# Performance work log

Measured on AMD Instinct MI355X. Metric: run time of the kernel, lower is better.

The kernel has to match this reference:

```python
import jax, jax.numpy as jnp
import numpy as np

N_HEADS = 16
DIM = 1024
HEAD_DIM = DIM // N_HEADS

def setup_inputs() -> dict:
    key = jax.random.key(0)
    ks = jax.random.split(key, 5)
    B, S = 4, 2048
    x = jax.random.normal(ks[0], (B, S, DIM), dtype=jnp.float32)
    # PyTorch Linear-style params (stored as [in, out] for x @ W)
    sc = 1.0 / np.sqrt(DIM)
    W_qkv = jax.random.uniform(ks[1], (DIM, 3 * DIM), jnp.float32, -sc, sc)
    b_qkv = jax.random.uniform(ks[2], (3 * DIM,), jnp.float32, -sc, sc)
    W_o = jax.random.uniform(ks[3], (DIM, DIM), jnp.float32, -sc, sc)
    b_o = jax.random.uniform(ks[4], (DIM,), jnp.float32, -sc, sc)
    return {"x": x, "W_qkv": W_qkv, "b_qkv": b_qkv, "W_o": W_o, "b_o": b_o}

def reference(x, W_qkv, b_qkv, W_o, b_o):
    B, S, D = x.shape
    qkv = x @ W_qkv + b_qkv                       # [B,S,3D]
    q, k, v = jnp.split(qkv, 3, axis=2)
    # [B,S,D] -> [B,H,S,hd]
    q = q.reshape(B, S, N_HEADS, HEAD_DIM).transpose(0, 2, 1, 3)
    k = k.reshape(B, S, N_HEADS, HEAD_DIM).transpose(0, 2, 1, 3)
    v = v.reshape(B, S, N_HEADS, HEAD_DIM).transpose(0, 2, 1, 3)
    aff = jnp.einsum('bhqd,bhkd->bhqk', q, k) / jnp.sqrt(jnp.float32(HEAD_DIM))
    causal = jnp.tril(jnp.ones((S, S), dtype=bool))  # [S,S]
    aff = jnp.where(causal[None, None], aff, jnp.float32(-jnp.inf))
    attn = jax.nn.softmax(aff, axis=3)
    # dropout p=0.0 (eval): identity
    out = jnp.einsum('bhqk,bhkd->bhqd', attn, v)
    out = out.transpose(0, 2, 1, 3).reshape(B, S, D)
    return out @ W_o + b_o
```

## Files before the change

### kernel.cpp

```cpp
#include <hip/hip_runtime.h>

typedef unsigned short u16;
typedef short bf16x8 __attribute__((ext_vector_type(8)));
typedef float f32x4 __attribute__((ext_vector_type(4)));
typedef unsigned short ushort8v __attribute__((ext_vector_type(8)));
typedef unsigned short us4 __attribute__((ext_vector_type(4)));
typedef float f4v __attribute__((ext_vector_type(4)));

#define LOG2E 1.4426950408889634f
#define FIXMAX_C (12.0f * LOG2E)

static __device__ __forceinline__ float bf2f(u16 h) {
    unsigned int u = ((unsigned int)h) << 16;
    return __builtin_bit_cast(float, u);
}
static __device__ __forceinline__ u16 f2bf(float f) {
    unsigned int u = __builtin_bit_cast(unsigned int, f);
    u += 0x7FFFu + ((u >> 16) & 1u);
    return (u16)(u >> 16);
}
static __device__ __forceinline__ void ld_lds16(const u16* g, u16* l) {
    __builtin_amdgcn_global_load_lds((const __attribute__((address_space(1))) void*)g,
                                     (__attribute__((address_space(3))) void*)l, 16, 0, 0);
}
#define MFMA16(a, b, c) __builtin_amdgcn_mfma_f32_16x16x32_bf16(a, b, c, 0, 0, 0)
#define SW(r, g) (((r) << 6) + ((((g) ^ ((r) & 7))) << 3))

__global__ void cvt_cast(const float* __restrict__ src, u16* __restrict__ dst, int n4) {
    int i = blockIdx.x * blockDim.x + threadIdx.x;
    const int stride = gridDim.x * blockDim.x;
    for (; i < n4; i += stride) {
        f4v v = *(const f4v*)(src + (size_t)i * 4);
        us4 o;
        o[0] = f2bf(v[0]); o[1] = f2bf(v[1]); o[2] = f2bf(v[2]); o[3] = f2bf(v[3]);
        *(us4*)(dst + (size_t)i * 4) = o;
    }
}

__global__ void cvt_T(const float* __restrict__ W, u16* __restrict__ WT, int N, int K) {
    int idx = blockIdx.x * 256 + threadIdx.x;
    int n = idx % N;
    int k0 = (idx / N) * 4;
    us4 pk;
    #pragma unroll
    for (int j = 0; j < 4; j++) pk[j] = f2bf(W[(size_t)(k0 + j) * N + n]);
    *(us4*)&WT[(size_t)n * K + k0] = pk;
}

template <int MODE>
__global__ __launch_bounds__(256) void gemm128(
        const u16* __restrict__ A, const u16* __restrict__ BT,
        const u16* __restrict__ bias, void* __restrict__ Cout,
        u16* __restrict__ vT, int K) {
    __shared__ u16 As[128 * 32];
    __shared__ u16 Bs[128 * 32];
    const int tid = threadIdx.x, lane = tid & 63, wid = tid >> 6;
    const int lm = lane & 15, q = lane >> 4;
    const int m0 = blockIdx.y * 128, n0 = blockIdx.x * 128;
    const int wm = (wid >> 1) * 64, wn = (wid & 1) * 64;
    f32x4 acc[4][4] = {};

    const int srow = wid * 32 + (lane >> 2);
    const int scol = (lane & 3) * 8;
    const u16* ga0 = A + (size_t)(m0 + srow) * K + scol;
    const u16* ga1 = ga0 + (size_t)16 * K;
    const u16* gb0 = BT + (size_t)(n0 + srow) * K + scol;
    const u16* gb1 = gb0 + (size_t)16 * K;
    u16* lA = &As[wid * 32 * 32];
    u16* lB = &Bs[wid * 32 * 32];

    for (int kb = 0; kb < K; kb += 32) {
        __syncthreads();
        ld_lds16(ga0 + kb, lA);
        ld_lds16(ga1 + kb, lA + 16 * 32);
        ld_lds16(gb0 + kb, lB);
        ld_lds16(gb1 + kb, lB + 16 * 32);
        __syncthreads();
        bf16x8 af[4], bfr[4];
        #pragma unroll
        for (int mi = 0; mi < 4; mi++) af[mi] = *(const bf16x8*)&As[(wm + mi * 16 + lm) * 32 + q * 8];
        #pragma unroll
        for (int ni = 0; ni < 4; ni++) bfr[ni] = *(const bf16x8*)&Bs[(wn + ni * 16 + lm) * 32 + q * 8];
        #pragma unroll
        for (int mi = 0; mi < 4; mi++)
            #pragma unroll
            for (int ni = 0; ni < 4; ni++)
                acc[mi][ni] = MFMA16(af[mi], bfr[ni], acc[mi][ni]);
    }

    if constexpr (MODE == 0) {
        u16* qkout = (u16*)Cout;
        if (n0 < 2048) {
            #pragma unroll
            for (int ni = 0; ni < 4; ni++) {
                int col = n0 + wn + ni * 16 + lm;
                float bsv = bf2f(bias[col]);
                float sc = (col < 1024) ? 0.125f : 1.0f;
                #pragma unroll
                for (int mi = 0; mi < 4; mi++)
                    #pragma unroll
                    for (int r = 0; r < 4; r++) {
                        int row = m0 + wm + mi * 16 + q * 4 + r;
                        qkout[(size_t)row * 2048 + col] = f2bf((acc[mi][ni][r] + bsv) * sc);
                    }
            }
        } else {
            const int b_ = m0 >> 11;
            const int sb = (m0 & 2047) + wm;
            #pragma unroll
            for (int ni = 0; ni < 4; ni++) {
                int col = n0 + wn + ni * 16 + lm;
                int hh = (col - 2048) >> 6, dd = (col - 2048) & 63;
                float bsv = bf2f(bias[col]);
                u16* dst = vT + ((size_t)((b_ * 16 + hh) * 64 + dd)) * 2048;
                #pragma unroll
                for (int mi = 0; mi < 4; mi++) {
                    us4 pk;
                    #pragma unroll
                    for (int r = 0; r < 4; r++) pk[r] = f2bf(acc[mi][ni][r] + bsv);
                    *(us4*)&dst[sb + mi * 16 + q * 4] = pk;
                }
            }
        }
    } else {
        float* out = (float*)Cout;
        #pragma unroll
        for (int ni = 0; ni < 4; ni++) {
            int col = n0 + wn + ni * 16 + lm;
            float bsv = bf2f(bias[col]);
            #pragma unroll
            for (int mi = 0; mi < 4; mi++)
                #pragma unroll
                for (int r = 0; r < 4; r++) {
                    int row = m0 + wm + mi * 16 + q * 4 + r;
                    out[(size_t)row * 1024 + col] = acc[mi][ni][r] + bsv;
                }
        }
    }
}

template <bool DIAG>
__device__ __forceinline__ void proc_tile(
        const bf16x8* qf, const u16* __restrict__ ksv, const u16* __restrict__ vsv,
        u16* __restrict__ psw, f32x4* o, f32x4& lacc, const bf16x8 ones,
        int lm, int q, int m0w) {
    f32x4 s[4] = {};
    #pragma unroll
    for (int g2 = 0; g2 < 2; g2++) {
        bf16x8 a = qf[g2];
        #pragma unroll
        for (int nt = 0; nt < 4; nt++) {
            bf16x8 bb = *(const bf16x8*)&ksv[SW(nt * 16 + lm, q + 4 * g2)];
            s[nt] = MFMA16(a, bb, s[nt]);
        }
    }
    #pragma unroll
    for (int nt = 0; nt < 4; nt++)
        #pragma unroll
        for (int r = 0; r < 4; r++) {
            float v = s[nt][r];
            if constexpr (DIAG) {
                if (nt * 16 + lm > m0w + q * 4 + r) v = -3e30f;
            }
            float pv = __builtin_amdgcn_exp2f(v * LOG2E - FIXMAX_C);
            psw[SW(q * 4 + r, 2 * nt + (lm >> 3)) + (lm & 7)] = f2bf(pv);
        }
    #pragma unroll
    for (int g2 = 0; g2 < 2; g2++) {
        bf16x8 ap = *(const bf16x8*)&psw[SW(lm, q + 4 * g2)];
        lacc = MFMA16(ap, ones, lacc);
        #pragma unroll
        for (int nt = 0; nt < 4; nt++) {
            bf16x8 bv = *(const bf16x8*)&vsv[SW(nt * 16 + lm, q + 4 * g2)];
            o[nt] = MFMA16(ap, bv, o[nt]);
        }
    }
}

__global__ __launch_bounds__(256, 2) void attn3(
        const u16* __restrict__ qk, const u16* __restrict__ vT, u16* __restrict__ aw) {
    __shared__ u16 smem[16384];
    u16* ks = smem;
    u16* vs = smem + 4096;
    const int tid = threadIdx.x, lane = tid & 63, wid = tid >> 6;
    const int lm = lane & 15, q = lane >> 4;
    const int bh = blockIdx.x, p = blockIdx.y;
    const int b = bh >> 4, h = bh & 15;
    const int t[4] = {p, 15 - p, 16 + p, 31 - p};
    const size_t rowbase = (size_t)b * 2048;
    const int lr = tid >> 2, lcg = (tid & 3) * 2, lc = (tid & 3) * 16;
    const int m0w = wid * 16;
    u16* psw = smem + 8192 + wid * 1024;

    bf16x8 ones;
    #pragma unroll
    for (int j = 0; j < 8; j++) ones[j] = (short)0x3F80;

    #pragma unroll
    for (int i = 0; i < 4; i++) {
        const u16* qa = qk + (rowbase + t[i] * 64 + lr) * 2048 + h * 64 + lc;
        *(ushort8v*)&smem[i * 4096 + SW(lr, lcg)]     = *(const ushort8v*)qa;
        *(ushort8v*)&smem[i * 4096 + SW(lr, lcg + 1)] = *(const ushort8v*)(qa + 8);
    }
    __syncthreads();
    bf16x8 qf[4][2];
    #pragma unroll
    for (int i = 0; i < 4; i++)
        #pragma unroll
        for (int g2 = 0; g2 < 2; g2++)
            qf[i][g2] = *(const bf16x8*)&smem[i * 4096 + SW(m0w + lm, q + 4 * g2)];

    f32x4 o[4][4] = {};
    f32x4 lacc[4] = {};

    const u16* kg = qk + (rowbase + lr) * 2048 + 1024 + h * 64 + lc;
    const u16* vg = vT + ((size_t)bh * 64 + lr) * 2048 + lc;
    const int jmax = t[3];

    ushort8v k0 = *(const ushort8v*)kg, k1 = *(const ushort8v*)(kg + 8);
    ushort8v v0 = *(const ushort8v*)vg, v1 = *(const ushort8v*)(vg + 8);

    for (int jt = 0; jt <= jmax; ++jt) {
        __syncthreads();
        *(ushort8v*)&ks[SW(lr, lcg)] = k0; *(ushort8v*)&ks[SW(lr, lcg + 1)] = k1;
        *(ushort8v*)&vs[SW(lr, lcg)] = v0; *(ushort8v*)&vs[SW(lr, lcg + 1)] = v1;
        __syncthreads();
        if (jt < jmax) {
            const u16* kgj = kg + (size_t)(jt + 1) * 64 * 2048;
            const u16* vgj = vg + (jt + 1) * 64;
            k0 = *(const ushort8v*)kgj; k1 = *(const ushort8v*)(kgj + 8);
            v0 = *(const ushort8v*)vgj; v1 = *(const ushort8v*)(vgj + 8);
        }
        #pragma unroll
        for (int i = 0; i < 4; i++) {
            if (jt < t[i])
                proc_tile<false>(qf[i], ks, vs, psw, o[i], lacc[i], ones, lm, q, m0w);
            else if (jt == t[i])
                proc_tile<true>(qf[i], ks, vs, psw, o[i], lacc[i], ones, lm, q, m0w);
        }
    }

    #pragma unroll
    for (int i = 0; i < 4; i++) {
        f32x4 li;
        #pragma unroll
        for (int r = 0; r < 4; r++) li[r] = __builtin_amdgcn_rcpf(lacc[i][r]);
        #pragma unroll
        for (int nt = 0; nt < 4; nt++)
            #pragma unroll
            for (int r = 0; r < 4; r++) {
                int row = t[i] * 64 + m0w + q * 4 + r;
                int col = h * 64 + nt * 16 + lm;
                aw[(rowbase + row) * 1024 + col] = f2bf(o[i][nt][r] * li[r]);
            }
    }
}

extern "C" void kernel_launch(void* const* d_in, const int* in_sizes, int n_in,
                              void* d_out, int out_size, void* d_ws, size_t ws_size,
                              hipStream_t stream) {
    const float* x    = (const float*)d_in[0];
    const float* Wqkv = (const float*)d_in[1];
    const float* bqkv = (const float*)d_in[2];
    const float* Wo   = (const float*)d_in[3];
    const float* bo   = (const float*)d_in[4];
    float* out = (float*)d_out;

    u16* xb     = (u16*)d_ws;
    u16* WqkvT  = xb + (size_t)8192 * 1024;
    u16* bqkvb  = WqkvT + (size_t)3072 * 1024;
    u16* WoT    = bqkvb + 3072;
    u16* bob    = WoT + (size_t)1024 * 1024;
    u16* qk     = bob + 1024;
    u16* vT     = qk + (size_t)8192 * 2048;
    u16* aw     = vT + (size_t)64 * 64 * 2048;

    cvt_cast<<<2048, 256, 0, stream>>>(x, xb, 8192 * 1024 / 4);
    cvt_cast<<<3,    256, 0, stream>>>(bqkv, bqkvb, 3072 / 4);
    cvt_cast<<<1,    256, 0, stream>>>(bo, bob, 1024 / 4);
    cvt_T<<<3072, 256, 0, stream>>>(Wqkv, WqkvT, 3072, 1024);
    cvt_T<<<1024, 256, 0, stream>>>(Wo, WoT, 1024, 1024);

    gemm128<0><<<dim3(24, 64), 256, 0, stream>>>(xb, WqkvT, bqkvb, qk, vT, 1024);
    attn3<<<dim3(64, 8), 256, 0, stream>>>(qk, vT, aw);
    gemm128<1><<<dim3(8, 64), 256, 0, stream>>>(aw, WoT, bob, out, nullptr, 1024);
}
```

Before: 296.1 us.

## Tile weight transpose through LDS, deepen GEMM K-step, add grouped block swizzle

The weight transpose-cast kernel now stages 64x64 tiles in shared memory, so both its global reads and writes are coalesced and vectorized instead of strided. The GEMM loads a 64-wide K chunk per barrier pair (two 32-wide LDS halves), which halves the number of synchronizations per tile. It also remaps the 1D block index into panels of 8 row-tiles to improve L2 reuse of the A and B tiles. This raises LDS use per GEMM block and adds index arithmetic.

```diff
diff --git a/kernel.cpp b/kernel.cpp
--- a/kernel.cpp
+++ b/kernel.cpp
@@ -37,55 +37,72 @@
     }
 }
 
-__global__ void cvt_T(const float* __restrict__ W, u16* __restrict__ WT, int N, int K) {
-    int idx = blockIdx.x * 256 + threadIdx.x;
-    int n = idx % N;
-    int k0 = (idx / N) * 4;
-    us4 pk;
-    #pragma unroll
-    for (int j = 0; j < 4; j++) pk[j] = f2bf(W[(size_t)(k0 + j) * N + n]);
-    *(us4*)&WT[(size_t)n * K + k0] = pk;
+__global__ __launch_bounds__(256) void cvt_T(const float* __restrict__ W, u16* __restrict__ WT,
+                                             int N, int K) {
+    __shared__ u16 tT[64][72];
+    const int tid = threadIdx.x;
+    const int tiles_n = N >> 6;
+    const int tn = blockIdx.x % tiles_n, tk = blockIdx.x / tiles_n;
+    const int rr = tid >> 4, c4 = (tid & 15) * 4;
+    #pragma unroll
+    for (int i = 0; i < 4; i++) {
+        int kk = rr + i * 16;
+        f4v v = *(const f4v*)&W[(size_t)(tk * 64 + kk) * N + tn * 64 + c4];
+        #pragma unroll
+        for (int j = 0; j < 4; j++) tT[c4 + j][kk] = f2bf(v[j]);
+    }
+    __syncthreads();
+    const int nrow = tid >> 2, kc = (tid & 3) * 16;
+    ushort8v a = *(const ushort8v*)&tT[nrow][kc];
+    ushort8v b = *(const ushort8v*)&tT[nrow][kc + 8];
+    u16* dst = WT + (size_t)(tn * 64 + nrow) * K + tk * 64 + kc;
+    *(ushort8v*)dst = a;
+    *(ushort8v*)(dst + 8) = b;
 }
 
 template <int MODE>
 __global__ __launch_bounds__(256) void gemm128(
         const u16* __restrict__ A, const u16* __restrict__ BT,
         const u16* __restrict__ bias, void* __restrict__ Cout,
-        u16* __restrict__ vT, int K) {
-    __shared__ u16 As[128 * 32];
-    __shared__ u16 Bs[128 * 32];
+        u16* __restrict__ vT, int K, int nx) {
+    __shared__ u16 As[2][128][32];
+    __shared__ u16 Bs[2][128][32];
     const int tid = threadIdx.x, lane = tid & 63, wid = tid >> 6;
     const int lm = lane & 15, q = lane >> 4;
-    const int m0 = blockIdx.y * 128, n0 = blockIdx.x * 128;
+    const int id = blockIdx.x;
+    const int panel = id / (nx * 8), rem = id % (nx * 8);
+    const int bx = rem >> 3, by = panel * 8 + (rem & 7);
+    const int m0 = by * 128, n0 = bx * 128;
     const int wm = (wid >> 1) * 64, wn = (wid & 1) * 64;
+    const int w32 = wid * 32;
     f32x4 acc[4][4] = {};
 
-    const int srow = wid * 32 + (lane >> 2);
-    const int scol = (lane & 3) * 8;
-    const u16* ga0 = A + (size_t)(m0 + srow) * K + scol;
-    const u16* ga1 = ga0 + (size_t)16 * K;
-    const u16* gb0 = BT + (size_t)(n0 + srow) * K + scol;
-    const u16* gb1 = gb0 + (size_t)16 * K;
-    u16* lA = &As[wid * 32 * 32];
-    u16* lB = &Bs[wid * 32 * 32];
-
-    for (int kb = 0; kb < K; kb += 32) {
+    const u16* gA = A + (size_t)(m0 + w32 + (lane >> 2)) * K + (lane & 3) * 8;
+    const u16* gB = BT + (size_t)(n0 + w32 + (lane >> 2)) * K + (lane & 3) * 8;
+
+    for (int kb = 0; kb < K; kb += 64) {
         __syncthreads();
-        ld_lds16(ga0 + kb, lA);
-        ld_lds16(ga1 + kb, lA + 16 * 32);
-        ld_lds16(gb0 + kb, lB);
-        ld_lds16(gb1 + kb, lB + 16 * 32);
+        #pragma unroll
+        for (int h = 0; h < 2; h++)
+            #pragma unroll
+            for (int i = 0; i < 2; i++) {
+                ld_lds16(gA + kb + h * 32 + (size_t)i * 16 * K, &As[h][w32 + i * 16][0]);
+                ld_lds16(gB + kb + h * 32 + (size_t)i * 16 * K, &Bs[h][w32 + i * 16][0]);
+            }
         __syncthreads();
-        bf16x8 af[4], bfr[4];
-        #pragma unroll
-        for (int mi = 0; mi < 4; mi++) af[mi] = *(const bf16x8*)&As[(wm + mi * 16 + lm) * 32 + q * 8];
-        #pragma unroll
-        for (int ni = 0; ni < 4; ni++) bfr[ni] = *(const bf16x8*)&Bs[(wn + ni * 16 + lm) * 32 + q * 8];
-        #pragma unroll
-        for (int mi = 0; mi < 4; mi++)
-            #pragma unroll
-            for (int ni = 0; ni < 4; ni++)
-                acc[mi][ni] = MFMA16(af[mi], bfr[ni], acc[mi][ni]);
+        #pragma unroll
+        for (int kk = 0; kk < 2; kk++) {
+            bf16x8 af[4], bfr[4];
+            #pragma unroll
+            for (int mi = 0; mi < 4; mi++) af[mi] = *(const bf16x8*)&As[kk][wm + mi * 16 + lm][q * 8];
+            #pragma unroll
+            for (int ni = 0; ni < 4; ni++) bfr[ni] = *(const bf16x8*)&Bs[kk][wn + ni * 16 + lm][q * 8];
+            #pragma unroll
+            for (int mi = 0; mi < 4; mi++)
+                #pragma unroll
+                for (int ni = 0; ni < 4; ni++)
+                    acc[mi][ni] = MFMA16(af[mi], bfr[ni], acc[mi][ni]);
+        }
     }
 
     if constexpr (MODE == 0) {
@@ -278,10 +295,10 @@
     cvt_cast<<<2048, 256, 0, stream>>>(x, xb, 8192 * 1024 / 4);
     cvt_cast<<<3,    256, 0, stream>>>(bqkv, bqkvb, 3072 / 4);
     cvt_cast<<<1,    256, 0, stream>>>(bo, bob, 1024 / 4);
-    cvt_T<<<3072, 256, 0, stream>>>(Wqkv, WqkvT, 3072, 1024);
-    cvt_T<<<1024, 256, 0, stream>>>(Wo, WoT, 1024, 1024);
-
-    gemm128<0><<<dim3(24, 64), 256, 0, stream>>>(xb, WqkvT, bqkvb, qk, vT, 1024);
+    cvt_T<<<48 * 16, 256, 0, stream>>>(Wqkv, WqkvT, 3072, 1024);
+    cvt_T<<<16 * 16, 256, 0, stream>>>(Wo, WoT, 1024, 1024);
+
+    gemm128<0><<<24 * 64, 256, 0, stream>>>(xb, WqkvT, bqkvb, qk, vT, 1024, 24);
     attn3<<<dim3(64, 8), 256, 0, stream>>>(qk, vT, aw);
-    gemm128<1><<<dim3(8, 64), 256, 0, stream>>>(aw, WoT, bob, out, nullptr, 1024);
-}
+    gemm128<1><<<8 * 64, 256, 0, stream>>>(aw, WoT, bob, out, nullptr, 1024, 8);
+}
```

New measurement: 275.1 us. -7.1%, faster.
